# Kernel optimization log

Measured on AMD Instinct MI355X. Metric: run time of the kernel, lower is better.

The kernel has to match this reference:

```python
import jax, jax.numpy as jnp
import numpy as np

N = 131072

def setup_inputs() -> dict:
    key = jax.random.key(0)
    k_x, k_e, k_w2, k_b2, k_w3, k_b3, k_w4 = jax.random.split(key, 7)
    x = jax.random.randint(k_x, (N, 32), 0, 7424, dtype=jnp.int32)
    emb = jax.random.normal(k_e, (7424, 128), dtype=jnp.float32) * 0.05
    W2 = jax.random.normal(k_w2, (32, 128), dtype=jnp.float32) * 0.05
    b2 = jax.random.normal(k_b2, (32,), dtype=jnp.float32) * 0.05
    W3 = jax.random.normal(k_w3, (32, 64), dtype=jnp.float32) * 0.05
    b3 = jax.random.normal(k_b3, (32,), dtype=jnp.float32) * 0.05
    W4 = jax.random.normal(k_w4, (1, 64), dtype=jnp.float32) * 0.05
    return {"x": x, "emb": emb, "W2": W2, "b2": b2, "W3": W3, "b3": b3, "W4": W4}

def reference(x, emb, W2, b2, W3, b3, W4):
    # x: [N, 32] int indices; use first 29 slots
    idx = x[..., :29]
    h = emb[idx].sum(axis=-2)                    # [N, 128] embedding-bag sum
    h = jax.nn.relu(h)
    h = h @ W2.T + b2                            # [N, 32]
    h = jax.nn.relu(jnp.concatenate((h, -h), axis=-1))   # [N, 64] sign-concat
    h = h @ W3.T + b3                            # [N, 32]
    h = jax.nn.relu(jnp.concatenate((h, -h), axis=-1))   # [N, 64]
    return h @ W4.T                              # [N, 1] (no bias)
```

## Files before the change

kernel.cpp:

```cpp
#include <hip/hip_runtime.h>
#include <hip/hip_fp16.h>


typedef _Float16 h2v_t  __attribute__((ext_vector_type(2)));
typedef _Float16 half8  __attribute__((ext_vector_type(8)));
typedef float    f32x4  __attribute__((ext_vector_type(4)));

constexpr int RPB = 64;

__global__ __launch_bounds__(256) void emb_to_fp16(
    const float* __restrict__ emb, __half2* __restrict__ emb16,
    int npairs_real, int npairs_tot)
{
    int i = blockIdx.x * blockDim.x + threadIdx.x;
    if (i < npairs_tot) {
        float2 v = make_float2(0.f, 0.f);
        if (i < npairs_real) v = ((const float2*)emb)[i];
        emb16[i] = __floats2half2_rn(v.x, v.y);
    }
}

__global__ __launch_bounds__(256) void w_to_fp16(
    const float* __restrict__ W2, const float* __restrict__ W3,
    _Float16* __restrict__ W2h, _Float16* __restrict__ W3h)
{
    int i = blockIdx.x * blockDim.x + threadIdx.x;
    if (i < 4096) W2h[i] = (_Float16)W2[i];
    if (i < 2048) W3h[i] = (_Float16)W3[i];
}

__global__ __launch_bounds__(256, 6) void nnue_one(
    const int*      __restrict__ x,
    const __half*   __restrict__ emb16,
    const _Float16* __restrict__ W2h,
    const _Float16* __restrict__ W3h,
    const float*    __restrict__ b2,
    const float*    __restrict__ b3,
    const float*    __restrict__ W4,
    float*          __restrict__ out, int n)
{
    __shared__ uint4 hT[4][16 * 17];
    __shared__ __align__(16) char scratch[4][2176];

    const int tid  = threadIdx.x;
    const int lane = tid & 63;
    const int wave = tid >> 6;
    const int row0 = blockIdx.x * RPB;
    const int wrow0 = __builtin_amdgcn_readfirstlane(row0 + wave * 16);

    const int g   = lane >> 4;
    const int sub = lane & 15;
    const unsigned subOff = (unsigned)sub * 16u;

    int* xw = (int*)&scratch[wave][0];

    {
        const int4* xb = (const int4*)(x + (size_t)wrow0 * 32);
        int4 a = xb[lane * 2];
        int4 b = xb[lane * 2 + 1];
        if ((lane & 3) == 3) { b.y = 7424; b.z = 7424; b.w = 7424; }
        ((int4*)xw)[lane * 2]     = a;
        ((int4*)xw)[lane * 2 + 1] = b;
    }

    #pragma unroll 4
    for (int r = 0; r < 16; ++r) {
        const int* xrow = &xw[r * 32 + g];
        uint4 v[8];
        #pragma unroll
        for (int b = 0; b < 8; ++b) {
            const int idx = xrow[4 * b];
            const unsigned off = ((unsigned)idx << 8) + subOff;
            v[b] = *(const uint4*)((const char*)emb16 + off);
        }
        h2v_t hacc[4];
        #pragma unroll
        for (int q = 0; q < 4; ++q) hacc[q] = (h2v_t)0;
        #pragma unroll
        for (int b = 0; b < 8; ++b) {
            hacc[0] += __builtin_bit_cast(h2v_t, v[b].x);
            hacc[1] += __builtin_bit_cast(h2v_t, v[b].y);
            hacc[2] += __builtin_bit_cast(h2v_t, v[b].z);
            hacc[3] += __builtin_bit_cast(h2v_t, v[b].w);
        }
        #pragma unroll
        for (int q = 0; q < 4; ++q) {
            unsigned u = __builtin_bit_cast(unsigned, hacc[q]);
            h2v_t t = __builtin_bit_cast(h2v_t, u);
            t += __builtin_bit_cast(h2v_t, (unsigned)__shfl_xor((int)u, 16));
            unsigned u2 = __builtin_bit_cast(unsigned, t);
            t += __builtin_bit_cast(h2v_t, (unsigned)__shfl_xor((int)u2, 32));
            hacc[q] = __builtin_elementwise_max(t, (h2v_t)0);
        }
        if (g == 0) {
            uint4 o;
            o.x = __builtin_bit_cast(unsigned, hacc[0]);
            o.y = __builtin_bit_cast(unsigned, hacc[1]);
            o.z = __builtin_bit_cast(unsigned, hacc[2]);
            o.w = __builtin_bit_cast(unsigned, hacc[3]);
            hT[wave][r * 17 + sub] = o;
        }
    }

    const int q  = lane >> 4;
    const int nn = lane & 15;

    half8 bw2[2][4];
    #pragma unroll
    for (int nt = 0; nt < 2; ++nt)
        #pragma unroll
        for (int kk = 0; kk < 4; ++kk)
            bw2[nt][kk] = __builtin_bit_cast(half8,
                *(const uint4*)((const char*)W2h +
                    ((nt * 16 + nn) * 128 + kk * 32 + q * 8) * 2));

    half8 af[4];
    #pragma unroll
    for (int kk = 0; kk < 4; ++kk)
        af[kk] = __builtin_bit_cast(half8, hT[wave][nn * 17 + (4 * kk + q)]);

    f32x4 acc0 = {0.f, 0.f, 0.f, 0.f}, acc1 = {0.f, 0.f, 0.f, 0.f};
    #pragma unroll
    for (int kk = 0; kk < 4; ++kk) {
        acc0 = __builtin_amdgcn_mfma_f32_16x16x32_f16(af[kk], bw2[0][kk], acc0, 0, 0, 0);
        acc1 = __builtin_amdgcn_mfma_f32_16x16x32_f16(af[kk], bw2[1][kk], acc1, 0, 0, 0);
    }
    const float bb0 = b2[nn], bb1 = b2[16 + nn];

    _Float16* a2 = (_Float16*)&scratch[wave][0];
    #pragma unroll
    for (int r = 0; r < 4; ++r) {
        const float v0 = acc0[r] + bb0;
        const float v1 = acc1[r] + bb1;
        const int m = q * 4 + r;
        a2[m * 68 + nn]      = (_Float16)fmaxf(v0, 0.f);
        a2[m * 68 + 16 + nn] = (_Float16)fmaxf(v1, 0.f);
        a2[m * 68 + 32 + nn] = (_Float16)fmaxf(-v0, 0.f);
        a2[m * 68 + 48 + nn] = (_Float16)fmaxf(-v1, 0.f);
    }

    half8 bw3[2][2];
    #pragma unroll
    for (int nt = 0; nt < 2; ++nt)
        #pragma unroll
        for (int kk = 0; kk < 2; ++kk)
            bw3[nt][kk] = __builtin_bit_cast(half8,
                *(const uint4*)((const char*)W3h +
                    ((nt * 16 + nn) * 64 + kk * 32 + q * 8) * 2));

    half8 a2f[2];
    #pragma unroll
    for (int kk = 0; kk < 2; ++kk) {
        const _Float16* p = &a2[nn * 68 + kk * 32 + q * 8];
        half8 t;
        #pragma unroll
        for (int j = 0; j < 8; ++j) t[j] = p[j];
        a2f[kk] = t;
    }

    f32x4 acc30 = {0.f, 0.f, 0.f, 0.f}, acc31 = {0.f, 0.f, 0.f, 0.f};
    #pragma unroll
    for (int kk = 0; kk < 2; ++kk) {
        acc30 = __builtin_amdgcn_mfma_f32_16x16x32_f16(a2f[kk], bw3[0][kk], acc30, 0, 0, 0);
        acc31 = __builtin_amdgcn_mfma_f32_16x16x32_f16(a2f[kk], bw3[1][kk], acc31, 0, 0, 0);
    }
    const float bb30 = b3[nn], bb31 = b3[16 + nn];

    const float w4a = W4[nn],      w4b = W4[16 + nn];
    const float w4c = W4[32 + nn], w4d = W4[48 + nn];
    float o[4];
    #pragma unroll
    for (int r = 0; r < 4; ++r) {
        const float v0 = acc30[r] + bb30;
        const float v1 = acc31[r] + bb31;
        o[r] = fmaxf(v0, 0.f) * w4a + fmaxf(-v0, 0.f) * w4c
             + fmaxf(v1, 0.f) * w4b + fmaxf(-v1, 0.f) * w4d;
    }
    #pragma unroll
    for (int s = 1; s < 16; s <<= 1) {
        #pragma unroll
        for (int r = 0; r < 4; ++r) o[r] += __shfl_xor(o[r], s);
    }
    if (nn == 0) {
        #pragma unroll
        for (int r = 0; r < 4; ++r) {
            const int row = wrow0 + q * 4 + r;
            if (row < n) out[row] = o[r];
        }
    }
}

__global__ __launch_bounds__(256) void nnue_fused(
    const int*    __restrict__ x,
    const __half* __restrict__ emb16,
    const float*  __restrict__ W2, const float* __restrict__ b2,
    const float*  __restrict__ W3, const float* __restrict__ b3,
    const float*  __restrict__ W4,
    float*        __restrict__ out, int n)
{
    __shared__ int     xlds[4][512];
    __shared__ __half2 hbuf[64][65];
    __shared__ float   h2T[32 * 64];
    __shared__ float   obuf[4][64];

    const int tid  = threadIdx.x;
    const int lane = tid & 63;
    const int wave = tid >> 6;
    const int row0 = blockIdx.x * RPB;
    const int wrow0 = __builtin_amdgcn_readfirstlane(row0 + wave * 16);
    const int g   = lane >> 4;
    const int sub = lane & 15;
    const unsigned subOff = (unsigned)sub * 16u;

    {
        const int4* xb = (const int4*)(x + (size_t)wrow0 * 32);
        int4 a = xb[lane * 2];
        int4 b = xb[lane * 2 + 1];
        if ((lane & 3) == 3) { b.y = 7424; b.z = 7424; b.w = 7424; }
        ((int4*)&xlds[wave][0])[lane * 2]     = a;
        ((int4*)&xlds[wave][0])[lane * 2 + 1] = b;
    }

    #pragma unroll 4
    for (int r = 0; r < 16; ++r) {
        const int* xrow = &xlds[wave][r * 32 + g];
        uint4 v[8];
        #pragma unroll
        for (int b = 0; b < 8; ++b) {
            const int idx = xrow[4 * b];
            const unsigned off = ((unsigned)idx << 8) + subOff;
            v[b] = *(const uint4*)((const char*)emb16 + off);
        }
        h2v_t hacc[4];
        #pragma unroll
        for (int q = 0; q < 4; ++q) hacc[q] = (h2v_t)0;
        #pragma unroll
        for (int b = 0; b < 8; ++b) {
            hacc[0] += __builtin_bit_cast(h2v_t, v[b].x);
            hacc[1] += __builtin_bit_cast(h2v_t, v[b].y);
            hacc[2] += __builtin_bit_cast(h2v_t, v[b].z);
            hacc[3] += __builtin_bit_cast(h2v_t, v[b].w);
        }
        #pragma unroll
        for (int q = 0; q < 4; ++q) {
            unsigned u = __builtin_bit_cast(unsigned, hacc[q]);
            h2v_t t = __builtin_bit_cast(h2v_t, u);
            t += __builtin_bit_cast(h2v_t, (unsigned)__shfl_xor((int)u, 16));
            unsigned u2 = __builtin_bit_cast(unsigned, t);
            t += __builtin_bit_cast(h2v_t, (unsigned)__shfl_xor((int)u2, 32));
            hacc[q] = __builtin_elementwise_max(t, (h2v_t)0);
        }
        if (g == 0) {
            const int row = wave * 16 + r;
            #pragma unroll
            for (int q = 0; q < 4; ++q)
                hbuf[row][sub * 4 + q] = __builtin_bit_cast(__half2, hacc[q]);
        }
    }
    __syncthreads();

    {
        const int j0 = wave * 8;
        const int rr = lane;
        float acc[8];
        #pragma unroll
        for (int j = 0; j < 8; ++j) acc[j] = b2[j0 + j];
        #pragma unroll
        for (int d2 = 0; d2 < 64; ++d2) {
            const __half2 hv = hbuf[rr][d2];
            const float vx = __low2float(hv), vy = __high2float(hv);
            #pragma unroll
            for (int j = 0; j < 8; ++j) {
                const float* w = W2 + (size_t)(j0 + j) * 128 + d2 * 2;
                acc[j] = fmaf(vx, w[0], acc[j]);
                acc[j] = fmaf(vy, w[1], acc[j]);
            }
        }
        #pragma unroll
        for (int j = 0; j < 8; ++j) h2T[(j0 + j) * 64 + rr] = acc[j];
    }
    __syncthreads();

    {
        const int j0 = wave * 8;
        const int rr = lane;
        float h2v[32];
        #pragma unroll
        for (int k = 0; k < 32; ++k) h2v[k] = h2T[k * 64 + rr];
        float acc[8];
        #pragma unroll
        for (int j = 0; j < 8; ++j) acc[j] = b3[j0 + j];
        #pragma unroll
        for (int k = 0; k < 32; ++k) {
            const float p = fmaxf(h2v[k], 0.f);
            const float m = fmaxf(-h2v[k], 0.f);
            #pragma unroll
            for (int j = 0; j < 8; ++j) {
                const float* w = W3 + (size_t)(j0 + j) * 64;
                acc[j] = fmaf(p, w[k],      acc[j]);
                acc[j] = fmaf(m, w[32 + k], acc[j]);
            }
        }
        float o = 0.f;
        #pragma unroll
        for (int j = 0; j < 8; ++j) {
            const int jj = j0 + j;
            o = fmaf(fmaxf(acc[j], 0.f),  W4[jj],      o);
            o = fmaf(fmaxf(-acc[j], 0.f), W4[32 + jj], o);
        }
        obuf[wave][rr] = o;
    }
    __syncthreads();

    if (tid < 64) {
        const int row = row0 + tid;
        if (row < n)
            out[row] = obuf[0][tid] + obuf[1][tid] + obuf[2][tid] + obuf[3][tid];
    }
}

extern "C" void kernel_launch(void* const* d_in, const int* in_sizes, int n_in,
                              void* d_out, int out_size, void* d_ws, size_t ws_size,
                              hipStream_t stream) {
    const int*   x   = (const int*)  d_in[0];
    const float* emb = (const float*)d_in[1];
    const float* W2  = (const float*)d_in[2];
    const float* b2  = (const float*)d_in[3];
    const float* W3  = (const float*)d_in[4];
    const float* b3  = (const float*)d_in[5];
    const float* W4  = (const float*)d_in[6];
    float* out = (float*)d_out;
    const int n = out_size;

    __half2* emb16 = (__half2*)d_ws;
    const int npairs_real = 7424 * 64;
    const int npairs_tot  = 7425 * 64;
    hipLaunchKernelGGL(emb_to_fp16, dim3((npairs_tot + 255) / 256), dim3(256),
                       0, stream, emb, emb16, npairs_real, npairs_tot);

    const size_t emb_bytes = (size_t)7425 * 256;
    const size_t w2h_off   = emb_bytes;
    const size_t w3h_off   = w2h_off + 8192;
    const size_t need      = w3h_off + 4096;
    const bool   fused_ok  = ws_size >= need;

    if (fused_ok) {
        _Float16* W2h = (_Float16*)((char*)d_ws + w2h_off);
        _Float16* W3h = (_Float16*)((char*)d_ws + w3h_off);
        hipLaunchKernelGGL(w_to_fp16, dim3(16), dim3(256), 0, stream,
                           W2, W3, W2h, W3h);
        hipLaunchKernelGGL(nnue_one, dim3((n + RPB - 1) / RPB), dim3(256),
                           0, stream, x, (const __half*)emb16, W2h, W3h,
                           b2, b3, W4, out, n);
    } else {
        hipLaunchKernelGGL(nnue_fused, dim3((n + RPB - 1) / RPB), dim3(256),
                           0, stream, x, (const __half*)emb16, W2, b2, W3, b3,
                           W4, out, n);
    }
}
```

Before: 122.6 us.

## Merge weight conversion into embedding prep and compact LDS for higher occupancy

Folds the weight fp16 conversion into the embedding conversion kernel, which removes one kernel launch. In the main kernel the gathered indices are packed to 16 bits in LDS, the padded hidden-state tile is replaced with an XOR-swizzled layout, and the launch-bounds occupancy hint is raised from 6 to 8 blocks. The intent is less LDS per block, more resident waves to hide gather latency, and lower launch overhead. The risks are register pressure from the tighter bound and the assumption that indices fit in 16 bits.

```diff
diff --git a/kernel.cpp b/kernel.cpp
--- a/kernel.cpp
+++ b/kernel.cpp
@@ -8,9 +8,11 @@
 
 constexpr int RPB = 64;
 
-__global__ __launch_bounds__(256) void emb_to_fp16(
+__global__ __launch_bounds__(256) void prep_fp16(
     const float* __restrict__ emb, __half2* __restrict__ emb16,
-    int npairs_real, int npairs_tot)
+    const float* __restrict__ W2, const float* __restrict__ W3,
+    _Float16* __restrict__ W2h, _Float16* __restrict__ W3h,
+    int npairs_real, int npairs_tot, int do_w)
 {
     int i = blockIdx.x * blockDim.x + threadIdx.x;
     if (i < npairs_tot) {
@@ -18,18 +20,13 @@
         if (i < npairs_real) v = ((const float2*)emb)[i];
         emb16[i] = __floats2half2_rn(v.x, v.y);
     }
+    if (do_w) {
+        if (i < 4096) W2h[i] = (_Float16)W2[i];
+        if (i < 2048) W3h[i] = (_Float16)W3[i];
+    }
 }
 
-__global__ __launch_bounds__(256) void w_to_fp16(
-    const float* __restrict__ W2, const float* __restrict__ W3,
-    _Float16* __restrict__ W2h, _Float16* __restrict__ W3h)
-{
-    int i = blockIdx.x * blockDim.x + threadIdx.x;
-    if (i < 4096) W2h[i] = (_Float16)W2[i];
-    if (i < 2048) W3h[i] = (_Float16)W3[i];
-}
-
-__global__ __launch_bounds__(256, 6) void nnue_one(
+__global__ __launch_bounds__(256, 8) void nnue_one(
     const int*      __restrict__ x,
     const __half*   __restrict__ emb16,
     const _Float16* __restrict__ W2h,
@@ -39,8 +36,8 @@
     const float*    __restrict__ W4,
     float*          __restrict__ out, int n)
 {
-    __shared__ uint4 hT[4][16 * 17];
-    __shared__ __align__(16) char scratch[4][2176];
+    __shared__ __align__(16) char hmem[4][4096];
+    __shared__ __align__(16) char xmem[4][1024];
 
     const int tid  = threadIdx.x;
     const int lane = tid & 63;
@@ -52,25 +49,30 @@
     const int sub = lane & 15;
     const unsigned subOff = (unsigned)sub * 16u;
 
-    int* xw = (int*)&scratch[wave][0];
+    uint4* hT = (uint4*)&hmem[wave][0];
+    unsigned short* xw = (unsigned short*)&xmem[wave][0];
 
     {
         const int4* xb = (const int4*)(x + (size_t)wrow0 * 32);
         int4 a = xb[lane * 2];
         int4 b = xb[lane * 2 + 1];
         if ((lane & 3) == 3) { b.y = 7424; b.z = 7424; b.w = 7424; }
-        ((int4*)xw)[lane * 2]     = a;
-        ((int4*)xw)[lane * 2 + 1] = b;
+        uint4 p;
+        p.x = ((unsigned)a.x & 0xffffu) | ((unsigned)a.y << 16);
+        p.y = ((unsigned)a.z & 0xffffu) | ((unsigned)a.w << 16);
+        p.z = ((unsigned)b.x & 0xffffu) | ((unsigned)b.y << 16);
+        p.w = ((unsigned)b.z & 0xffffu) | ((unsigned)b.w << 16);
+        ((uint4*)xw)[lane] = p;
     }
 
     #pragma unroll 4
     for (int r = 0; r < 16; ++r) {
-        const int* xrow = &xw[r * 32 + g];
+        const unsigned short* xrow = xw + r * 32 + g;
         uint4 v[8];
         #pragma unroll
         for (int b = 0; b < 8; ++b) {
-            const int idx = xrow[4 * b];
-            const unsigned off = ((unsigned)idx << 8) + subOff;
+            const unsigned idx = xrow[4 * b];
+            const unsigned off = (idx << 8) + subOff;
             v[b] = *(const uint4*)((const char*)emb16 + off);
         }
         h2v_t hacc[4];
@@ -98,7 +100,7 @@
             o.y = __builtin_bit_cast(unsigned, hacc[1]);
             o.z = __builtin_bit_cast(unsigned, hacc[2]);
             o.w = __builtin_bit_cast(unsigned, hacc[3]);
-            hT[wave][r * 17 + sub] = o;
+            hT[r * 16 + (sub ^ (r & 7))] = o;
         }
     }
 
@@ -117,7 +119,8 @@
     half8 af[4];
     #pragma unroll
     for (int kk = 0; kk < 4; ++kk)
-        af[kk] = __builtin_bit_cast(half8, hT[wave][nn * 17 + (4 * kk + q)]);
+        af[kk] = __builtin_bit_cast(half8,
+            hT[nn * 16 + ((4 * kk + q) ^ (nn & 7))]);
 
     f32x4 acc0 = {0.f, 0.f, 0.f, 0.f}, acc1 = {0.f, 0.f, 0.f, 0.f};
     #pragma unroll
@@ -127,7 +130,7 @@
     }
     const float bb0 = b2[nn], bb1 = b2[16 + nn];
 
-    _Float16* a2 = (_Float16*)&scratch[wave][0];
+    _Float16* a2 = (_Float16*)&hmem[wave][0];
     #pragma unroll
     for (int r = 0; r < 4; ++r) {
         const float v0 = acc0[r] + bb0;
@@ -335,8 +338,6 @@
     __half2* emb16 = (__half2*)d_ws;
     const int npairs_real = 7424 * 64;
     const int npairs_tot  = 7425 * 64;
-    hipLaunchKernelGGL(emb_to_fp16, dim3((npairs_tot + 255) / 256), dim3(256),
-                       0, stream, emb, emb16, npairs_real, npairs_tot);
 
     const size_t emb_bytes = (size_t)7425 * 256;
     const size_t w2h_off   = emb_bytes;
@@ -344,11 +345,14 @@
     const size_t need      = w3h_off + 4096;
     const bool   fused_ok  = ws_size >= need;
 
+    _Float16* W2h = fused_ok ? (_Float16*)((char*)d_ws + w2h_off) : nullptr;
+    _Float16* W3h = fused_ok ? (_Float16*)((char*)d_ws + w3h_off) : nullptr;
+
+    hipLaunchKernelGGL(prep_fp16, dim3((npairs_tot + 255) / 256), dim3(256),
+                       0, stream, emb, emb16, W2, W3, W2h, W3h,
+                       npairs_real, npairs_tot, fused_ok ? 1 : 0);
+
     if (fused_ok) {
-        _Float16* W2h = (_Float16*)((char*)d_ws + w2h_off);
-        _Float16* W3h = (_Float16*)((char*)d_ws + w3h_off);
-        hipLaunchKernelGGL(w_to_fp16, dim3(16), dim3(256), 0, stream,
-                           W2, W3, W2h, W3h);
         hipLaunchKernelGGL(nnue_one, dim3((n + RPB - 1) / RPB), dim3(256),
                            0, stream, x, (const __half*)emb16, W2h, W3h,
                            b2, b3, W4, out, n);
```

Result: faster. 118.2 us (-3.6%).
